# Performance work log

Measured on AMD Instinct MI355X. Metric: run time of the kernel, lower is better.

Reference implementation:

```python
import jax, jax.numpy as jnp
import numpy as np

B, N, C = 4, 1024, 768
H, K, TEMP = 12, 32, 1.0
D = C // H
EPS = 1e-9


def setup_inputs() -> dict:
    key = jax.random.key(0)
    ks = jax.random.split(key, 5)
    x = jax.random.normal(ks[0], (B, N, C), dtype=jnp.float32)
    u = jax.random.uniform(ks[1], (B, N, N), dtype=jnp.float32)
    qkv_w = jax.random.normal(ks[2], (C, 3 * C), dtype=jnp.float32) * 0.02
    qkv_b = jnp.zeros((3 * C,), dtype=jnp.float32)
    proj_w = jax.random.normal(ks[3], (C, C), dtype=jnp.float32) * 0.02
    proj_b = jnp.zeros((C,), dtype=jnp.float32)
    head_scores = jnp.ones((H,), dtype=jnp.float32)
    return {"x": x, "u": u, "qkv_w": qkv_w, "qkv_b": qkv_b,
            "proj_w": proj_w, "proj_b": proj_b, "head_scores": head_scores}


def reference(x, u, qkv_w, qkv_b, proj_w, proj_b, head_scores):
    # qkv projection: [B,N,3C] -> [3,B,H,N,D]
    qkv = (x @ qkv_w + qkv_b).reshape(B, N, 3, H, D)
    qkv = jnp.transpose(qkv, (2, 0, 3, 1, 4))
    q, k, v = qkv[0], qkv[1], qkv[2]

    scale = 1.0 / np.sqrt(D)
    # full dense scores [B,H,N,N] (torch computes this twice; same math once)
    scores = jnp.einsum('bhnd,bhmd->bhnm', q, k) * scale

    # Gumbel top-K gate over head-averaged logits
    logits = scores.mean(axis=1)                         # [B,N,N]
    gumbel = -jnp.log(-jnp.log(u + EPS) + EPS)
    probs = jax.nn.softmax((logits + gumbel) / TEMP, axis=-1)
    topk_vals = jax.lax.top_k(probs, K)[0]               # sorted descending
    thresh = topk_vals[..., -1:]                          # K-th largest
    sparse_mask = (probs >= thresh).astype(scores.dtype)  # [B,N,N]

    # post-softmax masking (breaks flash fusion)
    attn = jax.nn.softmax(scores, axis=-1) * sparse_mask[:, None]
    out = jnp.einsum('bhnm,bhmd->bhnd', attn, v)          # [B,H,N,D]
    out = jnp.transpose(out, (0, 2, 1, 3)).reshape(B, N, C)
    return (out * head_scores.mean()) @ proj_w + proj_b
```

## Files before the change

### kernel.cpp

```cpp
#include <hip/hip_runtime.h>
#include <hip/hip_bf16.h>
#include <math.h>

#define B_ 4
#define N_ 1024
#define C_ 768
#define H_ 12
#define D_ 64
#define TOPK_ 32
#define EPS_ 1e-9f

#define LDN_ 32
#define LK_  72
#define QKS_ 1536

typedef __attribute__((ext_vector_type(8))) short bf16x8;
typedef __attribute__((ext_vector_type(4))) float f32x4;
typedef unsigned short u16;

struct TopkRec { unsigned int cnt; unsigned short c[62]; };

__device__ __forceinline__ u16 f2bf(float f) {
    unsigned int u = __float_as_uint(f);
    u += 0x7fffu + ((u >> 16) & 1u);
    return (u16)(u >> 16);
}
__device__ __forceinline__ float bf2f(u16 h) {
    return __uint_as_float(((unsigned int)h) << 16);
}

__device__ __forceinline__ void gll16(const void* g, void* l) {
    __builtin_amdgcn_global_load_lds(
        (const __attribute__((address_space(1))) void*)g,
        (__attribute__((address_space(3))) void*)l, 16, 0, 0);
}

__global__ __launch_bounds__(256) void conv_x(
    const float* __restrict__ X, u16* __restrict__ Xh, u16* __restrict__ Xl)
{
    const size_t off = ((size_t)blockIdx.x * 256 + threadIdx.x) * 8;
    float4 a = *(const float4*)&X[off];
    float4 b = *(const float4*)&X[off + 4];
    float v[8] = {a.x, a.y, a.z, a.w, b.x, b.y, b.z, b.w};
    u16 hb[8], lb[8];
    #pragma unroll
    for (int i = 0; i < 8; ++i) {
        u16 hi = f2bf(v[i]);
        hb[i] = hi;
        lb[i] = f2bf(v[i] - bf2f(hi));
    }
    *(bf16x8*)&Xh[off] = *(const bf16x8*)&hb[0];
    *(bf16x8*)&Xl[off] = *(const bf16x8*)&lb[0];
}

__global__ __launch_bounds__(256) void conv_w_nt(
    const float* __restrict__ W, u16* __restrict__ Wt_h, u16* __restrict__ Wt_l,
    int Kdim, int Ncols)
{
    __shared__ float Ts[64][65];
    const int t  = threadIdx.x;
    const int r  = t >> 2;
    const int cq = (t & 3) * 16;
    const int n0 = blockIdx.x * 64, k0 = blockIdx.y * 64;

    #pragma unroll
    for (int q = 0; q < 4; ++q) {
        float4 v = *(const float4*)&W[(size_t)(k0 + r) * Ncols + n0 + cq + q * 4];
        Ts[r][cq + q * 4 + 0] = v.x;
        Ts[r][cq + q * 4 + 1] = v.y;
        Ts[r][cq + q * 4 + 2] = v.z;
        Ts[r][cq + q * 4 + 3] = v.w;
    }
    __syncthreads();
    u16 hb[16], lb[16];
    #pragma unroll
    for (int i = 0; i < 16; ++i) {
        float val = Ts[cq + i][r];
        u16 hi = f2bf(val);
        hb[i] = hi;
        lb[i] = f2bf(val - bf2f(hi));
    }
    const size_t obase = (size_t)(n0 + r) * Kdim + k0 + cq;
    *(bf16x8*)&Wt_h[obase]     = *(const bf16x8*)&hb[0];
    *(bf16x8*)&Wt_h[obase + 8] = *(const bf16x8*)&hb[8];
    *(bf16x8*)&Wt_l[obase]     = *(const bf16x8*)&lb[0];
    *(bf16x8*)&Wt_l[obase + 8] = *(const bf16x8*)&lb[8];
}

__global__ __launch_bounds__(256) void gemm_qkv(
    const u16* __restrict__ Ath, const u16* __restrict__ Atl,
    const u16* __restrict__ Bth, const u16* __restrict__ Btl,
    const float* __restrict__ bias,
    u16* __restrict__ Ch, u16* __restrict__ Cl, float* __restrict__ Vf)
{
    __shared__ u16 Ah[128 * LDN_], Al[128 * LDN_];
    __shared__ u16 Bh[128 * LDN_], Bl[128 * LDN_];
    const int t    = threadIdx.x;
    const int m0   = blockIdx.y * 128, n0 = blockIdx.x * 128;
    const int lane = t & 63, w = t >> 6;
    const int wm   = (w >> 1) * 64, wn = (w & 1) * 64;
    const int fr   = lane & 15, kg8 = lane >> 4;
    const int w16  = w * 16;
    const int r4s  = lane >> 2, q4s = (lane & 3) * 8;

    f32x4 acc[4][4];
    #pragma unroll
    for (int i = 0; i < 4; ++i)
        #pragma unroll
        for (int j = 0; j < 4; ++j)
            acc[i][j] = (f32x4){0.f, 0.f, 0.f, 0.f};

    for (int k0 = 0; k0 < C_; k0 += 32) {
        __syncthreads();
        {
            const size_t ga0 = (size_t)(m0 + w16 + r4s) * C_ + k0 + q4s;
            const size_t ga1 = ga0 + (size_t)64 * C_;
            const size_t gb0 = (size_t)(n0 + w16 + r4s) * C_ + k0 + q4s;
            const size_t gb1 = gb0 + (size_t)64 * C_;
            gll16(&Ath[ga0], &Ah[w16 * LDN_]);
            gll16(&Ath[ga1], &Ah[(64 + w16) * LDN_]);
            gll16(&Atl[ga0], &Al[w16 * LDN_]);
            gll16(&Atl[ga1], &Al[(64 + w16) * LDN_]);
            gll16(&Bth[gb0], &Bh[w16 * LDN_]);
            gll16(&Bth[gb1], &Bh[(64 + w16) * LDN_]);
            gll16(&Btl[gb0], &Bl[w16 * LDN_]);
            gll16(&Btl[gb1], &Bl[(64 + w16) * LDN_]);
        }
        __syncthreads();

        bf16x8 aF[4], bF[4], a2F[4], b2F[4];
        #pragma unroll
        for (int fm = 0; fm < 4; ++fm)
            aF[fm] = *(const bf16x8*)&Ah[(wm + fm * 16 + fr) * LDN_ + kg8 * 8];
        #pragma unroll
        for (int fn = 0; fn < 4; ++fn)
            bF[fn] = *(const bf16x8*)&Bh[(wn + fn * 16 + fr) * LDN_ + kg8 * 8];
        #pragma unroll
        for (int fm = 0; fm < 4; ++fm)
            #pragma unroll
            for (int fn = 0; fn < 4; ++fn)
                acc[fm][fn] = __builtin_amdgcn_mfma_f32_16x16x32_bf16(
                    aF[fm], bF[fn], acc[fm][fn], 0, 0, 0);
        #pragma unroll
        for (int fn = 0; fn < 4; ++fn)
            b2F[fn] = *(const bf16x8*)&Bl[(wn + fn * 16 + fr) * LDN_ + kg8 * 8];
        #pragma unroll
        for (int fm = 0; fm < 4; ++fm)
            #pragma unroll
            for (int fn = 0; fn < 4; ++fn)
                acc[fm][fn] = __builtin_amdgcn_mfma_f32_16x16x32_bf16(
                    aF[fm], b2F[fn], acc[fm][fn], 0, 0, 0);
        #pragma unroll
        for (int fm = 0; fm < 4; ++fm)
            a2F[fm] = *(const bf16x8*)&Al[(wm + fm * 16 + fr) * LDN_ + kg8 * 8];
        #pragma unroll
        for (int fm = 0; fm < 4; ++fm)
            #pragma unroll
            for (int fn = 0; fn < 4; ++fn)
                acc[fm][fn] = __builtin_amdgcn_mfma_f32_16x16x32_bf16(
                    a2F[fm], bF[fn], acc[fm][fn], 0, 0, 0);
    }

    const int r4 = (lane >> 4) * 4;
    const bool isV = (n0 >= 1536);
    #pragma unroll
    for (int fn = 0; fn < 4; ++fn) {
        const int col = n0 + wn + fn * 16 + fr;
        const float bv = bias[col];
        #pragma unroll
        for (int fm = 0; fm < 4; ++fm)
            #pragma unroll
            for (int i = 0; i < 4; ++i) {
                const int rown = m0 + wm + fm * 16 + r4 + i;
                float val = acc[fm][fn][i] + bv;
                if (isV) {
                    Vf[(size_t)rown * C_ + col - 1536] = val;
                } else {
                    const size_t o = (size_t)rown * QKS_ + col;
                    u16 hi = f2bf(val);
                    Ch[o] = hi;
                    Cl[o] = f2bf(val - bf2f(hi));
                }
            }
    }
}

__global__ __launch_bounds__(256) void attn_fused(
    const u16* __restrict__ qh, const u16* __restrict__ ql,
    const float* __restrict__ u, float* __restrict__ z,
    float2* __restrict__ mlp)
{
    __shared__ u16 KsH[128 * LK_], KsL[128 * LK_];

    const int t    = threadIdx.x;
    const int lane = t & 63, w = t >> 6;
    const int fr   = lane & 15, kg8 = lane >> 4;
    const int n0   = blockIdx.x * 64;
    const int m0   = blockIdx.y * 128;
    const int mc   = blockIdx.y;
    const int b    = blockIdx.z;

    f32x4 zacc[8];
    #pragma unroll
    for (int fn = 0; fn < 8; ++fn) zacc[fn] = (f32x4){0.f, 0.f, 0.f, 0.f};

    const int kr = t >> 1, kd = (t & 1) * 32;

    for (int hd = 0; hd < H_; ++hd) {
        const size_t qb = (size_t)(b * N_ + n0 + w * 16 + fr) * QKS_ + hd * 64 + kg8 * 8;
        bf16x8 aH0 = *(const bf16x8*)&qh[qb];
        bf16x8 aH1 = *(const bf16x8*)&qh[qb + 32];
        bf16x8 aL0 = *(const bf16x8*)&ql[qb];
        bf16x8 aL1 = *(const bf16x8*)&ql[qb + 32];

        const size_t kb = (size_t)(b * N_ + m0 + kr) * QKS_ + 768 + hd * 64 + kd;
        bf16x8 h0 = *(const bf16x8*)&qh[kb];
        bf16x8 h1 = *(const bf16x8*)&qh[kb + 8];
        bf16x8 h2 = *(const bf16x8*)&qh[kb + 16];
        bf16x8 h3 = *(const bf16x8*)&qh[kb + 24];
        bf16x8 l0 = *(const bf16x8*)&ql[kb];
        bf16x8 l1 = *(const bf16x8*)&ql[kb + 8];
        bf16x8 l2 = *(const bf16x8*)&ql[kb + 16];
        bf16x8 l3 = *(const bf16x8*)&ql[kb + 24];

        __syncthreads();
        const int sb = kr * LK_ + kd;
        *(bf16x8*)&KsH[sb]      = h0;  *(bf16x8*)&KsH[sb + 8]  = h1;
        *(bf16x8*)&KsH[sb + 16] = h2;  *(bf16x8*)&KsH[sb + 24] = h3;
        *(bf16x8*)&KsL[sb]      = l0;  *(bf16x8*)&KsL[sb + 8]  = l1;
        *(bf16x8*)&KsL[sb + 16] = l2;  *(bf16x8*)&KsL[sb + 24] = l3;
        __syncthreads();

        f32x4 acc[8];
        #pragma unroll
        for (int fn = 0; fn < 8; ++fn) acc[fn] = (f32x4){0.f, 0.f, 0.f, 0.f};

        #pragma unroll
        for (int fn = 0; fn < 8; ++fn) {
            const int bidx = (fn * 16 + fr) * LK_ + kg8 * 8;
            bf16x8 bH = *(const bf16x8*)&KsH[bidx];
            bf16x8 bL = *(const bf16x8*)&KsL[bidx];
            acc[fn] = __builtin_amdgcn_mfma_f32_16x16x32_bf16(aH0, bH, acc[fn], 0, 0, 0);
            acc[fn] = __builtin_amdgcn_mfma_f32_16x16x32_bf16(aH0, bL, acc[fn], 0, 0, 0);
            acc[fn] = __builtin_amdgcn_mfma_f32_16x16x32_bf16(aL0, bH, acc[fn], 0, 0, 0);
        }
        #pragma unroll
        for (int fn = 0; fn < 8; ++fn) {
            const int bidx = (fn * 16 + fr) * LK_ + 32 + kg8 * 8;
            bf16x8 bH = *(const bf16x8*)&KsH[bidx];
            bf16x8 bL = *(const bf16x8*)&KsL[bidx];
            acc[fn] = __builtin_amdgcn_mfma_f32_16x16x32_bf16(aH1, bH, acc[fn], 0, 0, 0);
            acc[fn] = __builtin_amdgcn_mfma_f32_16x16x32_bf16(aH1, bL, acc[fn], 0, 0, 0);
            acc[fn] = __builtin_amdgcn_mfma_f32_16x16x32_bf16(aL1, bH, acc[fn], 0, 0, 0);
        }

        #pragma unroll
        for (int fn = 0; fn < 8; ++fn) {
            zacc[fn][0] += acc[fn][0];
            zacc[fn][1] += acc[fn][1];
            zacc[fn][2] += acc[fn][2];
            zacc[fn][3] += acc[fn][3];
        }

        #pragma unroll
        for (int reg = 0; reg < 4; ++reg) {
            float tmax = acc[0][reg];
            #pragma unroll
            for (int fn = 1; fn < 8; ++fn) tmax = fmaxf(tmax, acc[fn][reg]);
            tmax *= 0.125f;
            tmax = fmaxf(tmax, __shfl_xor(tmax, 1));
            tmax = fmaxf(tmax, __shfl_xor(tmax, 2));
            tmax = fmaxf(tmax, __shfl_xor(tmax, 4));
            tmax = fmaxf(tmax, __shfl_xor(tmax, 8));
            float tsum = 0.f;
            #pragma unroll
            for (int fn = 0; fn < 8; ++fn)
                tsum += expf(acc[fn][reg] * 0.125f - tmax);
            tsum += __shfl_xor(tsum, 1);
            tsum += __shfl_xor(tsum, 2);
            tsum += __shfl_xor(tsum, 4);
            tsum += __shfl_xor(tsum, 8);
            if (fr == 0) {
                const int n = n0 + w * 16 + kg8 * 4 + reg;
                mlp[(((size_t)(b * H_ + hd)) * N_ + n) * 8 + mc] =
                    make_float2(tmax, tsum);
            }
        }
    }

    const float sc = 0.125f / 12.0f;
    #pragma unroll
    for (int fn = 0; fn < 8; ++fn) {
        const int m = m0 + fn * 16 + fr;
        #pragma unroll
        for (int reg = 0; reg < 4; ++reg) {
            const int n = n0 + w * 16 + kg8 * 4 + reg;
            const float uv = u[((size_t)(b * N_ + n)) * N_ + m];
            const float g  = -logf(-logf(uv + EPS_) + EPS_);
            z[((size_t)(b * N_ + n)) * N_ + m] = zacc[fn][reg] * sc + g;
        }
    }
}

__global__ __launch_bounds__(256) void ml_merge(
    const float2* __restrict__ mlp, float2* __restrict__ ml)
{
    const size_t idx = (size_t)blockIdx.x * 256 + threadIdx.x;
    float2 p[8];
    #pragma unroll
    for (int i = 0; i < 8; ++i) p[i] = mlp[idx * 8 + i];
    float m = p[0].x;
    #pragma unroll
    for (int i = 1; i < 8; ++i) m = fmaxf(m, p[i].x);
    float l = 0.f;
    #pragma unroll
    for (int i = 0; i < 8; ++i) l += p[i].y * expf(p[i].x - m);
    ml[idx] = make_float2(m, l);
}

__global__ __launch_bounds__(64) void topk_cols_kernel(
    const float* __restrict__ z, TopkRec* __restrict__ recs)
{
    const int row  = blockIdx.x;
    const int lane = threadIdx.x;
    const float* zr = z + (size_t)row * N_;
    float zv[16], wk[16];
    #pragma unroll
    for (int j = 0; j < 16; ++j) { zv[j] = zr[lane + 64 * j]; wk[j] = zv[j]; }

    float thresh = -INFINITY;
    for (int it = 0; it < TOPK_; ++it) {
        float lm = wk[0]; int li = 0;
        #pragma unroll
        for (int j = 1; j < 16; ++j)
            if (wk[j] > lm) { lm = wk[j]; li = j; }
        float gm = lm;
        gm = fmaxf(gm, __shfl_xor(gm, 1));
        gm = fmaxf(gm, __shfl_xor(gm, 2));
        gm = fmaxf(gm, __shfl_xor(gm, 4));
        gm = fmaxf(gm, __shfl_xor(gm, 8));
        gm = fmaxf(gm, __shfl_xor(gm, 16));
        gm = fmaxf(gm, __shfl_xor(gm, 32));
        unsigned long long has = __ballot(lm == gm);
        int first = __ffsll((unsigned long long)has) - 1;
        if (lane == first) wk[li] = -INFINITY;
        thresh = gm;
    }

    const unsigned long long below = ((unsigned long long)1 << lane) - 1;
    unsigned int basec = 0;
    TopkRec* rec = recs + row;
    #pragma unroll
    for (int j = 0; j < 16; ++j) {
        unsigned long long wmask = __ballot(zv[j] >= thresh);
        if (zv[j] >= thresh) {
            unsigned int pos = basec + (unsigned int)__popcll(wmask & below);
            if (pos < 62u) rec->c[pos] = (unsigned short)(lane + 64 * j);
        }
        basec += (unsigned int)__popcll(wmask);
    }
    if (lane == 0) rec->cnt = basec > 62u ? 62u : basec;
}

__global__ __launch_bounds__(256) void sparse_pv_kernel(
    const u16* __restrict__ qh, const u16* __restrict__ ql,
    const float* __restrict__ Vf,
    const TopkRec* __restrict__ recs, const float2* __restrict__ ml,
    const float* __restrict__ head_scores,
    u16* __restrict__ out1h, u16* __restrict__ out1l)
{
    __shared__ int cols_s[62];
    __shared__ int cnt_s;

    const int t    = threadIdx.x;
    const int lane = t & 63, wv = t >> 6;
    const int c4   = lane >> 2;
    const int dq   = lane & 3;
    const int row  = blockIdx.x;
    const int b    = row >> 10, n = row & 1023;

    const TopkRec* rec = recs + row;
    if (t == 0) cnt_s = (int)min(rec->cnt, 62u);
    if (t < 62) cols_s[t] = rec->c[t];

    float hsum = 0.f;
    #pragma unroll
    for (int i = 0; i < H_; ++i) hsum += head_scores[i];
    const float hs_mean = hsum * (1.0f / 12.0f);
    __syncthreads();
    const int cnt = cnt_s;
    const int nbatch = (cnt + 15) >> 4;

    for (int hd = wv; hd < H_; hd += 4) {
        float qv[16];
        {
            const size_t qb = (size_t)row * QKS_ + hd * 64 + dq * 16;
            bf16x8 qh0 = *(const bf16x8*)&qh[qb], qh1 = *(const bf16x8*)&qh[qb + 8];
            bf16x8 ql0 = *(const bf16x8*)&ql[qb], ql1 = *(const bf16x8*)&ql[qb + 8];
            #pragma unroll
            for (int i = 0; i < 8; ++i) {
                qv[i]     = bf2f((u16)qh0[i]) + bf2f((u16)ql0[i]);
                qv[i + 8] = bf2f((u16)qh1[i]) + bf2f((u16)ql1[i]);
            }
        }
        const float2 mlv = ml[((size_t)(b * H_ + hd)) * N_ + n];

        float acc[16];
        #pragma unroll
        for (int i = 0; i < 16; ++i) acc[i] = 0.f;

        for (int batch = 0; batch < nbatch; ++batch) {
            const int cidx  = batch * 16 + c4;
            const bool valid = (cidx < cnt);
            const int col   = cols_s[valid ? cidx : cnt - 1];

            const size_t kb = (size_t)(b * N_ + col) * QKS_ + 768 + hd * 64 + dq * 16;
            bf16x8 kh0 = *(const bf16x8*)&qh[kb], kh1 = *(const bf16x8*)&qh[kb + 8];
            bf16x8 kl0 = *(const bf16x8*)&ql[kb], kl1 = *(const bf16x8*)&ql[kb + 8];
            float dot = 0.f;
            #pragma unroll
            for (int i = 0; i < 8; ++i) {
                dot += qv[i]     * (bf2f((u16)kh0[i]) + bf2f((u16)kl0[i]));
                dot += qv[i + 8] * (bf2f((u16)kh1[i]) + bf2f((u16)kl1[i]));
            }
            dot += __shfl_xor(dot, 1);
            dot += __shfl_xor(dot, 2);
            float p = valid ? expf(dot * 0.125f - mlv.x) : 0.f;

            const float* vb = &Vf[(size_t)(b * N_ + col) * C_ + hd * 64 + dq * 16];
            #pragma unroll
            for (int q = 0; q < 4; ++q) {
                float4 v4 = *(const float4*)&vb[q * 4];
                acc[q * 4 + 0] += p * v4.x;
                acc[q * 4 + 1] += p * v4.y;
                acc[q * 4 + 2] += p * v4.z;
                acc[q * 4 + 3] += p * v4.w;
            }
        }

        #pragma unroll
        for (int d = 4; d < 64; d <<= 1)
            #pragma unroll
            for (int i = 0; i < 16; ++i)
                acc[i] += __shfl_xor(acc[i], d);

        if (c4 == 0) {
            const float s = hs_mean / mlv.y;
            u16 hb[16], lb[16];
            #pragma unroll
            for (int i = 0; i < 16; ++i) {
                float val = acc[i] * s;
                u16 hi = f2bf(val);
                hb[i] = hi;
                lb[i] = f2bf(val - bf2f(hi));
            }
            const size_t ob = (size_t)row * C_ + hd * 64 + dq * 16;
            *(bf16x8*)&out1h[ob]     = *(const bf16x8*)&hb[0];
            *(bf16x8*)&out1h[ob + 8] = *(const bf16x8*)&hb[8];
            *(bf16x8*)&out1l[ob]     = *(const bf16x8*)&lb[0];
            *(bf16x8*)&out1l[ob + 8] = *(const bf16x8*)&lb[8];
        }
    }
}

__global__ __launch_bounds__(256) void gemm_proj(
    const u16* __restrict__ Ath, const u16* __restrict__ Atl,
    const u16* __restrict__ Bth, const u16* __restrict__ Btl,
    const float* __restrict__ bias, float* __restrict__ Cm)
{
    __shared__ u16 Ah[128 * LDN_], Al[128 * LDN_];
    __shared__ u16 Bh[128 * LDN_], Bl[128 * LDN_];
    const int t    = threadIdx.x;
    const int m0   = blockIdx.y * 128, n0 = blockIdx.x * 128;
    const int lane = t & 63, w = t >> 6;
    const int wm   = (w >> 1) * 64, wn = (w & 1) * 64;
    const int fr   = lane & 15, kg8 = lane >> 4;
    const int w16  = w * 16;
    const int r4s  = lane >> 2, q4s = (lane & 3) * 8;

    f32x4 acc[4][4];
    #pragma unroll
    for (int i = 0; i < 4; ++i)
        #pragma unroll
        for (int j = 0; j < 4; ++j)
            acc[i][j] = (f32x4){0.f, 0.f, 0.f, 0.f};

    for (int k0 = 0; k0 < C_; k0 += 32) {
        __syncthreads();
        {
            const size_t ga0 = (size_t)(m0 + w16 + r4s) * C_ + k0 + q4s;
            const size_t ga1 = ga0 + (size_t)64 * C_;
            const size_t gb0 = (size_t)(n0 + w16 + r4s) * C_ + k0 + q4s;
            const size_t gb1 = gb0 + (size_t)64 * C_;
            gll16(&Ath[ga0], &Ah[w16 * LDN_]);
            gll16(&Ath[ga1], &Ah[(64 + w16) * LDN_]);
            gll16(&Atl[ga0], &Al[w16 * LDN_]);
            gll16(&Atl[ga1], &Al[(64 + w16) * LDN_]);
            gll16(&Bth[gb0], &Bh[w16 * LDN_]);
            gll16(&Bth[gb1], &Bh[(64 + w16) * LDN_]);
            gll16(&Btl[gb0], &Bl[w16 * LDN_]);
            gll16(&Btl[gb1], &Bl[(64 + w16) * LDN_]);
        }
        __syncthreads();

        bf16x8 aF[4], bF[4], a2F[4], b2F[4];
        #pragma unroll
        for (int fm = 0; fm < 4; ++fm)
            aF[fm] = *(const bf16x8*)&Ah[(wm + fm * 16 + fr) * LDN_ + kg8 * 8];
        #pragma unroll
        for (int fn = 0; fn < 4; ++fn)
            bF[fn] = *(const bf16x8*)&Bh[(wn + fn * 16 + fr) * LDN_ + kg8 * 8];
        #pragma unroll
        for (int fm = 0; fm < 4; ++fm)
            #pragma unroll
            for (int fn = 0; fn < 4; ++fn)
                acc[fm][fn] = __builtin_amdgcn_mfma_f32_16x16x32_bf16(
                    aF[fm], bF[fn], acc[fm][fn], 0, 0, 0);
        #pragma unroll
        for (int fn = 0; fn < 4; ++fn)
            b2F[fn] = *(const bf16x8*)&Bl[(wn + fn * 16 + fr) * LDN_ + kg8 * 8];
        #pragma unroll
        for (int fm = 0; fm < 4; ++fm)
            #pragma unroll
            for (int fn = 0; fn < 4; ++fn)
                acc[fm][fn] = __builtin_amdgcn_mfma_f32_16x16x32_bf16(
                    aF[fm], b2F[fn], acc[fm][fn], 0, 0, 0);
        #pragma unroll
        for (int fm = 0; fm < 4; ++fm)
            a2F[fm] = *(const bf16x8*)&Al[(wm + fm * 16 + fr) * LDN_ + kg8 * 8];
        #pragma unroll
        for (int fm = 0; fm < 4; ++fm)
            #pragma unroll
            for (int fn = 0; fn < 4; ++fn)
                acc[fm][fn] = __builtin_amdgcn_mfma_f32_16x16x32_bf16(
                    a2F[fm], bF[fn], acc[fm][fn], 0, 0, 0);
    }

    const int r4 = (lane >> 4) * 4;
    #pragma unroll
    for (int fn = 0; fn < 4; ++fn) {
        const int col = n0 + wn + fn * 16 + fr;
        const float bv = bias[col];
        #pragma unroll
        for (int fm = 0; fm < 4; ++fm)
            #pragma unroll
            for (int i = 0; i < 4; ++i)
                Cm[(size_t)(m0 + wm + fm * 16 + r4 + i) * C_ + col] =
                    acc[fm][fn][i] + bv;
    }
}

extern "C" void kernel_launch(void* const* d_in, const int* in_sizes, int n_in,
                              void* d_out, int out_size, void* d_ws, size_t ws_size,
                              hipStream_t stream)
{
    (void)in_sizes; (void)n_in; (void)out_size; (void)ws_size;
    const float* x           = (const float*)d_in[0];
    const float* u           = (const float*)d_in[1];
    const float* qkv_w       = (const float*)d_in[2];
    const float* qkv_b       = (const float*)d_in[3];
    const float* proj_w      = (const float*)d_in[4];
    const float* proj_b      = (const float*)d_in[5];
    const float* head_scores = (const float*)d_in[6];
    float* out = (float*)d_out;

    char* ws = (char*)d_ws;
    u16*     qkv_h  = (u16*)ws;
    u16*     qkv_l  = (u16*)(ws + 12582912);
    float*   Vf     = (float*)(ws + 25165824);
    char*    R      = ws + 37748736;
    u16*     wq_t_h = (u16*)R;
    u16*     wq_t_l = (u16*)(R + 3538944);
    float*   z      = (float*)R;
    TopkRec* recs   = (TopkRec*)(R + 16777216);
    u16*     wp_t_h = (u16*)R;
    u16*     wp_t_l = (u16*)(R + 1179648);
    float2*  ml     = (float2*)(R + 2359296);
    u16*     out1h  = (u16*)(R + 2752512);
    u16*     out1l  = (u16*)(R + 9043968);
    u16*     x_h    = (u16*)d_out;
    u16*     x_l    = (u16*)((char*)d_out + 6291456);
    float2*  mlp    = (float2*)d_out;

    conv_x<<<dim3(4096 * 768 / 8 / 256), dim3(256), 0, stream>>>(x, x_h, x_l);

    conv_w_nt<<<dim3(2304 / 64, 768 / 64), dim3(256), 0, stream>>>(
        qkv_w, wq_t_h, wq_t_l, 768, 2304);

    gemm_qkv<<<dim3(2304 / 128, 4096 / 128), dim3(256), 0, stream>>>(
        x_h, x_l, wq_t_h, wq_t_l, qkv_b, qkv_h, qkv_l, Vf);

    attn_fused<<<dim3(16, 8, B_), dim3(256), 0, stream>>>(
        qkv_h, qkv_l, u, z, mlp);

    topk_cols_kernel<<<dim3(B_ * N_), dim3(64), 0, stream>>>(z, recs);

    conv_w_nt<<<dim3(768 / 64, 768 / 64), dim3(256), 0, stream>>>(
        proj_w, wp_t_h, wp_t_l, 768, 768);

    ml_merge<<<dim3(B_ * H_ * N_ / 256), dim3(256), 0, stream>>>(mlp, ml);

    sparse_pv_kernel<<<dim3(B_ * N_), dim3(256), 0, stream>>>(
        qkv_h, qkv_l, Vf, recs, ml, head_scores, out1h, out1l);

    gemm_proj<<<dim3(768 / 128, 4096 / 128), dim3(256), 0, stream>>>(
        out1h, out1l, wp_t_h, wp_t_l, proj_b, out);
}
```

Baseline: 290.8 us.

## Double-buffer LDS tiles in QKV/proj GEMMs and remap blocks per XCD

Both split-bf16 GEMMs now use two LDS buffers, issuing the async global→LDS loads for the next K tile before computing on the current one, with one barrier per iteration instead of two. Block indices are also remapped so that blocks landing on the same XCD cover a contiguous region of output tiles, which is meant to improve L2 reuse. The cost is double the shared memory (64 KB per block), which may reduce occupancy. Correctness also depends on the async LDS writes being complete at the single barrier.

After: 293.3 us. About the same (+0.8%).

```diff
diff --git a/kernel.cpp b/kernel.cpp
--- a/kernel.cpp
+++ b/kernel.cpp
@@ -13,6 +13,7 @@
 #define LDN_ 32
 #define LK_  72
 #define QKS_ 1536
+#define HBUF_ (128 * LDN_)
 
 typedef __attribute__((ext_vector_type(8))) short bf16x8;
 typedef __attribute__((ext_vector_type(4))) float f32x4;
@@ -93,48 +94,58 @@
     const float* __restrict__ bias,
     u16* __restrict__ Ch, u16* __restrict__ Cl, float* __restrict__ Vf)
 {
-    __shared__ u16 Ah[128 * LDN_], Al[128 * LDN_];
-    __shared__ u16 Bh[128 * LDN_], Bl[128 * LDN_];
+    __shared__ u16 Ah[2 * HBUF_], Al[2 * HBUF_];
+    __shared__ u16 Bh[2 * HBUF_], Bl[2 * HBUF_];
     const int t    = threadIdx.x;
-    const int m0   = blockIdx.y * 128, n0 = blockIdx.x * 128;
+    const int d    = blockIdx.x;
+    const int xcd  = d & 7, j = d >> 3;
+    const int xt   = (xcd & 1) * 9 + (j % 9);
+    const int yt   = (xcd >> 1) * 8 + (j / 9);
+    const int m0   = yt * 128, n0 = xt * 128;
     const int lane = t & 63, w = t >> 6;
     const int wm   = (w >> 1) * 64, wn = (w & 1) * 64;
     const int fr   = lane & 15, kg8 = lane >> 4;
     const int w16  = w * 16;
     const int r4s  = lane >> 2, q4s = (lane & 3) * 8;
 
+    auto stage = [&](int k0, int buf) {
+        const int off = buf * HBUF_;
+        const size_t ga0 = (size_t)(m0 + w16 + r4s) * C_ + k0 + q4s;
+        const size_t ga1 = ga0 + (size_t)64 * C_;
+        const size_t gb0 = (size_t)(n0 + w16 + r4s) * C_ + k0 + q4s;
+        const size_t gb1 = gb0 + (size_t)64 * C_;
+        gll16(&Ath[ga0], &Ah[off + w16 * LDN_]);
+        gll16(&Ath[ga1], &Ah[off + (64 + w16) * LDN_]);
+        gll16(&Atl[ga0], &Al[off + w16 * LDN_]);
+        gll16(&Atl[ga1], &Al[off + (64 + w16) * LDN_]);
+        gll16(&Bth[gb0], &Bh[off + w16 * LDN_]);
+        gll16(&Bth[gb1], &Bh[off + (64 + w16) * LDN_]);
+        gll16(&Btl[gb0], &Bl[off + w16 * LDN_]);
+        gll16(&Btl[gb1], &Bl[off + (64 + w16) * LDN_]);
+    };
+
     f32x4 acc[4][4];
     #pragma unroll
     for (int i = 0; i < 4; ++i)
         #pragma unroll
-        for (int j = 0; j < 4; ++j)
-            acc[i][j] = (f32x4){0.f, 0.f, 0.f, 0.f};
-
-    for (int k0 = 0; k0 < C_; k0 += 32) {
-        __syncthreads();
-        {
-            const size_t ga0 = (size_t)(m0 + w16 + r4s) * C_ + k0 + q4s;
-            const size_t ga1 = ga0 + (size_t)64 * C_;
-            const size_t gb0 = (size_t)(n0 + w16 + r4s) * C_ + k0 + q4s;
-            const size_t gb1 = gb0 + (size_t)64 * C_;
-            gll16(&Ath[ga0], &Ah[w16 * LDN_]);
-            gll16(&Ath[ga1], &Ah[(64 + w16) * LDN_]);
-            gll16(&Atl[ga0], &Al[w16 * LDN_]);
-            gll16(&Atl[ga1], &Al[(64 + w16) * LDN_]);
-            gll16(&Bth[gb0], &Bh[w16 * LDN_]);
-            gll16(&Bth[gb1], &Bh[(64 + w16) * LDN_]);
-            gll16(&Btl[gb0], &Bl[w16 * LDN_]);
-            gll16(&Btl[gb1], &Bl[(64 + w16) * LDN_]);
-        }
-        __syncthreads();
-
+        for (int j2 = 0; j2 < 4; ++j2)
+            acc[i][j2] = (f32x4){0.f, 0.f, 0.f, 0.f};
+
+    stage(0, 0);
+    __syncthreads();
+    int cur = 0;
+
+    for (int kt = 0; kt < 24; ++kt) {
+        if (kt < 23) stage((kt + 1) * 32, cur ^ 1);
+
+        const int off = cur * HBUF_;
         bf16x8 aF[4], bF[4], a2F[4], b2F[4];
         #pragma unroll
         for (int fm = 0; fm < 4; ++fm)
-            aF[fm] = *(const bf16x8*)&Ah[(wm + fm * 16 + fr) * LDN_ + kg8 * 8];
+            aF[fm] = *(const bf16x8*)&Ah[off + (wm + fm * 16 + fr) * LDN_ + kg8 * 8];
         #pragma unroll
         for (int fn = 0; fn < 4; ++fn)
-            bF[fn] = *(const bf16x8*)&Bh[(wn + fn * 16 + fr) * LDN_ + kg8 * 8];
+            bF[fn] = *(const bf16x8*)&Bh[off + (wn + fn * 16 + fr) * LDN_ + kg8 * 8];
         #pragma unroll
         for (int fm = 0; fm < 4; ++fm)
             #pragma unroll
@@ -143,7 +154,7 @@
                     aF[fm], bF[fn], acc[fm][fn], 0, 0, 0);
         #pragma unroll
         for (int fn = 0; fn < 4; ++fn)
-            b2F[fn] = *(const bf16x8*)&Bl[(wn + fn * 16 + fr) * LDN_ + kg8 * 8];
+            b2F[fn] = *(const bf16x8*)&Bl[off + (wn + fn * 16 + fr) * LDN_ + kg8 * 8];
         #pragma unroll
         for (int fm = 0; fm < 4; ++fm)
             #pragma unroll
@@ -152,13 +163,16 @@
                     aF[fm], b2F[fn], acc[fm][fn], 0, 0, 0);
         #pragma unroll
         for (int fm = 0; fm < 4; ++fm)
-            a2F[fm] = *(const bf16x8*)&Al[(wm + fm * 16 + fr) * LDN_ + kg8 * 8];
+            a2F[fm] = *(const bf16x8*)&Al[off + (wm + fm * 16 + fr) * LDN_ + kg8 * 8];
         #pragma unroll
         for (int fm = 0; fm < 4; ++fm)
             #pragma unroll
             for (int fn = 0; fn < 4; ++fn)
                 acc[fm][fn] = __builtin_amdgcn_mfma_f32_16x16x32_bf16(
                     a2F[fm], bF[fn], acc[fm][fn], 0, 0, 0);
+
+        __syncthreads();
+        cur ^= 1;
     }
 
     const int r4 = (lane >> 4) * 4;
@@ -468,48 +482,58 @@
     const u16* __restrict__ Bth, const u16* __restrict__ Btl,
     const float* __restrict__ bias, float* __restrict__ Cm)
 {
-    __shared__ u16 Ah[128 * LDN_], Al[128 * LDN_];
-    __shared__ u16 Bh[128 * LDN_], Bl[128 * LDN_];
+    __shared__ u16 Ah[2 * HBUF_], Al[2 * HBUF_];
+    __shared__ u16 Bh[2 * HBUF_], Bl[2 * HBUF_];
     const int t    = threadIdx.x;
-    const int m0   = blockIdx.y * 128, n0 = blockIdx.x * 128;
+    const int d    = blockIdx.x;
+    const int xcd  = d & 7, j = d >> 3;
+    const int xt   = j % 6;
+    const int yt   = xcd * 4 + (j / 6);
+    const int m0   = yt * 128, n0 = xt * 128;
     const int lane = t & 63, w = t >> 6;
     const int wm   = (w >> 1) * 64, wn = (w & 1) * 64;
     const int fr   = lane & 15, kg8 = lane >> 4;
     const int w16  = w * 16;
     const int r4s  = lane >> 2, q4s = (lane & 3) * 8;
 
+    auto stage = [&](int k0, int buf) {
+        const int off = buf * HBUF_;
+        const size_t ga0 = (size_t)(m0 + w16 + r4s) * C_ + k0 + q4s;
+        const size_t ga1 = ga0 + (size_t)64 * C_;
+        const size_t gb0 = (size_t)(n0 + w16 + r4s) * C_ + k0 + q4s;
+        const size_t gb1 = gb0 + (size_t)64 * C_;
+        gll16(&Ath[ga0], &Ah[off + w16 * LDN_]);
+        gll16(&Ath[ga1], &Ah[off + (64 + w16) * LDN_]);
+        gll16(&Atl[ga0], &Al[off + w16 * LDN_]);
+        gll16(&Atl[ga1], &Al[off + (64 + w16) * LDN_]);
+        gll16(&Bth[gb0], &Bh[off + w16 * LDN_]);
+        gll16(&Bth[gb1], &Bh[off + (64 + w16) * LDN_]);
+        gll16(&Btl[gb0], &Bl[off + w16 * LDN_]);
+        gll16(&Btl[gb1], &Bl[off + (64 + w16) * LDN_]);
+    };
+
     f32x4 acc[4][4];
     #pragma unroll
     for (int i = 0; i < 4; ++i)
         #pragma unroll
-        for (int j = 0; j < 4; ++j)
-            acc[i][j] = (f32x4){0.f, 0.f, 0.f, 0.f};
-
-    for (int k0 = 0; k0 < C_; k0 += 32) {
-        __syncthreads();
-        {
-            const size_t ga0 = (size_t)(m0 + w16 + r4s) * C_ + k0 + q4s;
-            const size_t ga1 = ga0 + (size_t)64 * C_;
-            const size_t gb0 = (size_t)(n0 + w16 + r4s) * C_ + k0 + q4s;
-            const size_t gb1 = gb0 + (size_t)64 * C_;
-            gll16(&Ath[ga0], &Ah[w16 * LDN_]);
-            gll16(&Ath[ga1], &Ah[(64 + w16) * LDN_]);
-            gll16(&Atl[ga0], &Al[w16 * LDN_]);
-            gll16(&Atl[ga1], &Al[(64 + w16) * LDN_]);
-            gll16(&Bth[gb0], &Bh[w16 * LDN_]);
-            gll16(&Bth[gb1], &Bh[(64 + w16) * LDN_]);
-            gll16(&Btl[gb0], &Bl[w16 * LDN_]);
-            gll16(&Btl[gb1], &Bl[(64 + w16) * LDN_]);
-        }
-        __syncthreads();
-
+        for (int j2 = 0; j2 < 4; ++j2)
+            acc[i][j2] = (f32x4){0.f, 0.f, 0.f, 0.f};
+
+    stage(0, 0);
+    __syncthreads();
+    int cur = 0;
+
+    for (int kt = 0; kt < 24; ++kt) {
+        if (kt < 23) stage((kt + 1) * 32, cur ^ 1);
+
+        const int off = cur * HBUF_;
         bf16x8 aF[4], bF[4], a2F[4], b2F[4];
         #pragma unroll
         for (int fm = 0; fm < 4; ++fm)
-            aF[fm] = *(const bf16x8*)&Ah[(wm + fm * 16 + fr) * LDN_ + kg8 * 8];
+            aF[fm] = *(const bf16x8*)&Ah[off + (wm + fm * 16 + fr) * LDN_ + kg8 * 8];
         #pragma unroll
         for (int fn = 0; fn < 4; ++fn)
-            bF[fn] = *(const bf16x8*)&Bh[(wn + fn * 16 + fr) * LDN_ + kg8 * 8];
+            bF[fn] = *(const bf16x8*)&Bh[off + (wn + fn * 16 + fr) * LDN_ + kg8 * 8];
         #pragma unroll
         for (int fm = 0; fm < 4; ++fm)
             #pragma unroll
@@ -518,7 +542,7 @@
                     aF[fm], bF[fn], acc[fm][fn], 0, 0, 0);
         #pragma unroll
         for (int fn = 0; fn < 4; ++fn)
-            b2F[fn] = *(const bf16x8*)&Bl[(wn + fn * 16 + fr) * LDN_ + kg8 * 8];
+            b2F[fn] = *(const bf16x8*)&Bl[off + (wn + fn * 16 + fr) * LDN_ + kg8 * 8];
         #pragma unroll
         for (int fm = 0; fm < 4; ++fm)
             #pragma unroll
@@ -527,13 +551,16 @@
                     aF[fm], b2F[fn], acc[fm][fn], 0, 0, 0);
         #pragma unroll
         for (int fm = 0; fm < 4; ++fm)
-            a2F[fm] = *(const bf16x8*)&Al[(wm + fm * 16 + fr) * LDN_ + kg8 * 8];
+            a2F[fm] = *(const bf16x8*)&Al[off + (wm + fm * 16 + fr) * LDN_ + kg8 * 8];
         #pragma unroll
         for (int fm = 0; fm < 4; ++fm)
             #pragma unroll
             for (int fn = 0; fn < 4; ++fn)
                 acc[fm][fn] = __builtin_amdgcn_mfma_f32_16x16x32_bf16(
                     a2F[fm], bF[fn], acc[fm][fn], 0, 0, 0);
+
+        __syncthreads();
+        cur ^= 1;
     }
 
     const int r4 = (lane >> 4) * 4;
@@ -587,7 +614,7 @@
     conv_w_nt<<<dim3(2304 / 64, 768 / 64), dim3(256), 0, stream>>>(
         qkv_w, wq_t_h, wq_t_l, 768, 2304);
 
-    gemm_qkv<<<dim3(2304 / 128, 4096 / 128), dim3(256), 0, stream>>>(
+    gemm_qkv<<<dim3(576), dim3(256), 0, stream>>>(
         x_h, x_l, wq_t_h, wq_t_l, qkv_b, qkv_h, qkv_l, Vf);
 
     attn_fused<<<dim3(16, 8, B_), dim3(256), 0, stream>>>(
@@ -603,6 +630,6 @@
     sparse_pv_kernel<<<dim3(B_ * N_), dim3(256), 0, stream>>>(
         qkv_h, qkv_l, Vf, recs, ml, head_scores, out1h, out1l);
 
-    gemm_proj<<<dim3(768 / 128, 4096 / 128), dim3(256), 0, stream>>>(
+    gemm_proj<<<dim3(192), dim3(256), 0, stream>>>(
         out1h, out1l, wp_t_h, wp_t_l, proj_b, out);
 }
```

## Remap GEMM tiles per XCD and stage epilogue through LDS for vector stores

Applied to the files above, without the earlier changes.

Both projection GEMMs now use a 1D grid with a block-to-tile mapping that groups neighbouring output tiles on the same XCD, aiming for better L2 reuse of A/B panels. The epilogue writes accumulators into per-wave padded LDS staging, then each lane emits 16-byte vectorized global stores instead of scattered scalar 2-byte/4-byte stores. This adds an extra LDS round-trip and a barrier, and the GEMMs are a small part of total time.

After: 280.1 us. -3.7%, faster.

```diff
diff --git a/kernel.cpp b/kernel.cpp
--- a/kernel.cpp
+++ b/kernel.cpp
@@ -93,10 +93,18 @@
     const float* __restrict__ bias,
     u16* __restrict__ Ch, u16* __restrict__ Cl, float* __restrict__ Vf)
 {
-    __shared__ u16 Ah[128 * LDN_], Al[128 * LDN_];
-    __shared__ u16 Bh[128 * LDN_], Bl[128 * LDN_];
+    __shared__ __align__(16) char smem[34816];
+    u16* Ah = (u16*)(smem);
+    u16* Al = (u16*)(smem + 8192);
+    u16* Bh = (u16*)(smem + 16384);
+    u16* Bl = (u16*)(smem + 24576);
+
     const int t    = threadIdx.x;
-    const int m0   = blockIdx.y * 128, n0 = blockIdx.x * 128;
+    const int d    = blockIdx.x;
+    const int xcd  = d & 7, j = d >> 3;
+    const int xt   = (xcd & 1) * 9 + (j % 9);
+    const int yt   = (xcd >> 1) * 8 + (j / 9);
+    const int m0   = yt * 128, n0 = xt * 128;
     const int lane = t & 63, w = t >> 6;
     const int wm   = (w >> 1) * 64, wn = (w & 1) * 64;
     const int fr   = lane & 15, kg8 = lane >> 4;
@@ -107,10 +115,11 @@
     #pragma unroll
     for (int i = 0; i < 4; ++i)
         #pragma unroll
-        for (int j = 0; j < 4; ++j)
-            acc[i][j] = (f32x4){0.f, 0.f, 0.f, 0.f};
-
-    for (int k0 = 0; k0 < C_; k0 += 32) {
+        for (int j2 = 0; j2 < 4; ++j2)
+            acc[i][j2] = (f32x4){0.f, 0.f, 0.f, 0.f};
+
+    for (int kt = 0; kt < 24; ++kt) {
+        const int k0 = kt * 32;
         __syncthreads();
         {
             const size_t ga0 = (size_t)(m0 + w16 + r4s) * C_ + k0 + q4s;
@@ -160,28 +169,51 @@
                 acc[fm][fn] = __builtin_amdgcn_mfma_f32_16x16x32_bf16(
                     a2F[fm], bF[fn], acc[fm][fn], 0, 0, 0);
     }
-
-    const int r4 = (lane >> 4) * 4;
+    __syncthreads();
+
     const bool isV = (n0 >= 1536);
-    #pragma unroll
-    for (int fn = 0; fn < 4; ++fn) {
-        const int col = n0 + wn + fn * 16 + fr;
-        const float bv = bias[col];
-        #pragma unroll
-        for (int fm = 0; fm < 4; ++fm)
-            #pragma unroll
-            for (int i = 0; i < 4; ++i) {
-                const int rown = m0 + wm + fm * 16 + r4 + i;
-                float val = acc[fm][fn][i] + bv;
-                if (isV) {
-                    Vf[(size_t)rown * C_ + col - 1536] = val;
-                } else {
-                    const size_t o = (size_t)rown * QKS_ + col;
-                    u16 hi = f2bf(val);
-                    Ch[o] = hi;
-                    Cl[o] = f2bf(val - bf2f(hi));
+    float* Ts = (float*)(smem + w * 8448);
+    const int lr8 = lane >> 3, lc8 = (lane & 7) * 8;
+    #pragma unroll
+    for (int p = 0; p < 2; ++p) {
+        #pragma unroll
+        for (int fmh = 0; fmh < 2; ++fmh) {
+            const int fm = p * 2 + fmh;
+            #pragma unroll
+            for (int fn = 0; fn < 4; ++fn) {
+                const float bv = bias[n0 + wn + fn * 16 + fr];
+                #pragma unroll
+                for (int i = 0; i < 4; ++i)
+                    Ts[(fmh * 16 + kg8 * 4 + i) * 66 + fn * 16 + fr] =
+                        acc[fm][fn][i] + bv;
+            }
+        }
+        #pragma unroll
+        for (int it = 0; it < 4; ++it) {
+            const int r = it * 8 + lr8;
+            float v[8];
+            #pragma unroll
+            for (int c = 0; c < 8; ++c) v[c] = Ts[r * 66 + lc8 + c];
+            const int grow = m0 + wm + p * 32 + r;
+            const int gcol = n0 + wn + lc8;
+            if (isV) {
+                float4 v0 = {v[0], v[1], v[2], v[3]};
+                float4 v1 = {v[4], v[5], v[6], v[7]};
+                float* vp = &Vf[(size_t)grow * C_ + gcol - 1536];
+                *(float4*)vp       = v0;
+                *(float4*)(vp + 4) = v1;
+            } else {
+                u16 hb[8], lb[8];
+                #pragma unroll
+                for (int c = 0; c < 8; ++c) {
+                    u16 hi = f2bf(v[c]);
+                    hb[c] = hi;
+                    lb[c] = f2bf(v[c] - bf2f(hi));
                 }
-            }
+                *(bf16x8*)&Ch[(size_t)grow * QKS_ + gcol] = *(const bf16x8*)&hb[0];
+                *(bf16x8*)&Cl[(size_t)grow * QKS_ + gcol] = *(const bf16x8*)&lb[0];
+            }
+        }
     }
 }
 
@@ -468,10 +500,18 @@
     const u16* __restrict__ Bth, const u16* __restrict__ Btl,
     const float* __restrict__ bias, float* __restrict__ Cm)
 {
-    __shared__ u16 Ah[128 * LDN_], Al[128 * LDN_];
-    __shared__ u16 Bh[128 * LDN_], Bl[128 * LDN_];
+    __shared__ __align__(16) char smem[34816];
+    u16* Ah = (u16*)(smem);
+    u16* Al = (u16*)(smem + 8192);
+    u16* Bh = (u16*)(smem + 16384);
+    u16* Bl = (u16*)(smem + 24576);
+
     const int t    = threadIdx.x;
-    const int m0   = blockIdx.y * 128, n0 = blockIdx.x * 128;
+    const int d    = blockIdx.x;
+    const int xcd  = d & 7, j = d >> 3;
+    const int xt   = j % 6;
+    const int yt   = xcd * 4 + (j / 6);
+    const int m0   = yt * 128, n0 = xt * 128;
     const int lane = t & 63, w = t >> 6;
     const int wm   = (w >> 1) * 64, wn = (w & 1) * 64;
     const int fr   = lane & 15, kg8 = lane >> 4;
@@ -482,10 +522,11 @@
     #pragma unroll
     for (int i = 0; i < 4; ++i)
         #pragma unroll
-        for (int j = 0; j < 4; ++j)
-            acc[i][j] = (f32x4){0.f, 0.f, 0.f, 0.f};
-
-    for (int k0 = 0; k0 < C_; k0 += 32) {
+        for (int j2 = 0; j2 < 4; ++j2)
+            acc[i][j2] = (f32x4){0.f, 0.f, 0.f, 0.f};
+
+    for (int kt = 0; kt < 24; ++kt) {
+        const int k0 = kt * 32;
         __syncthreads();
         {
             const size_t ga0 = (size_t)(m0 + w16 + r4s) * C_ + k0 + q4s;
@@ -535,18 +576,38 @@
                 acc[fm][fn] = __builtin_amdgcn_mfma_f32_16x16x32_bf16(
                     a2F[fm], bF[fn], acc[fm][fn], 0, 0, 0);
     }
-
-    const int r4 = (lane >> 4) * 4;
-    #pragma unroll
-    for (int fn = 0; fn < 4; ++fn) {
-        const int col = n0 + wn + fn * 16 + fr;
-        const float bv = bias[col];
-        #pragma unroll
-        for (int fm = 0; fm < 4; ++fm)
-            #pragma unroll
-            for (int i = 0; i < 4; ++i)
-                Cm[(size_t)(m0 + wm + fm * 16 + r4 + i) * C_ + col] =
-                    acc[fm][fn][i] + bv;
+    __syncthreads();
+
+    float* Ts = (float*)(smem + w * 8448);
+    const int lr8 = lane >> 3, lc8 = (lane & 7) * 8;
+    #pragma unroll
+    for (int p = 0; p < 2; ++p) {
+        #pragma unroll
+        for (int fmh = 0; fmh < 2; ++fmh) {
+            const int fm = p * 2 + fmh;
+            #pragma unroll
+            for (int fn = 0; fn < 4; ++fn) {
+                const float bv = bias[n0 + wn + fn * 16 + fr];
+                #pragma unroll
+                for (int i = 0; i < 4; ++i)
+                    Ts[(fmh * 16 + kg8 * 4 + i) * 66 + fn * 16 + fr] =
+                        acc[fm][fn][i] + bv;
+            }
+        }
+        #pragma unroll
+        for (int it = 0; it < 4; ++it) {
+            const int r = it * 8 + lr8;
+            float v[8];
+            #pragma unroll
+            for (int c = 0; c < 8; ++c) v[c] = Ts[r * 66 + lc8 + c];
+            const int grow = m0 + wm + p * 32 + r;
+            const int gcol = n0 + wn + lc8;
+            float4 v0 = {v[0], v[1], v[2], v[3]};
+            float4 v1 = {v[4], v[5], v[6], v[7]};
+            float* cp = &Cm[(size_t)grow * C_ + gcol];
+            *(float4*)cp       = v0;
+            *(float4*)(cp + 4) = v1;
+        }
     }
 }
 
@@ -587,7 +648,7 @@
     conv_w_nt<<<dim3(2304 / 64, 768 / 64), dim3(256), 0, stream>>>(
         qkv_w, wq_t_h, wq_t_l, 768, 2304);
 
-    gemm_qkv<<<dim3(2304 / 128, 4096 / 128), dim3(256), 0, stream>>>(
+    gemm_qkv<<<dim3(576), dim3(256), 0, stream>>>(
         x_h, x_l, wq_t_h, wq_t_l, qkv_b, qkv_h, qkv_l, Vf);
 
     attn_fused<<<dim3(16, 8, B_), dim3(256), 0, stream>>>(
@@ -603,6 +664,6 @@
     sparse_pv_kernel<<<dim3(B_ * N_), dim3(256), 0, stream>>>(
         qkv_h, qkv_l, Vf, recs, ml, head_scores, out1h, out1l);
 
-    gemm_proj<<<dim3(768 / 128, 4096 / 128), dim3(256), 0, stream>>>(
+    gemm_proj<<<dim3(192), dim3(256), 0, stream>>>(
         out1h, out1l, wp_t_h, wp_t_l, proj_b, out);
 }
```
